# Kernel optimization log

Hardware: AMD Instinct MI355X
Metric: run time of the kernel (lower is better)

## Reference

```python
import jax, jax.numpy as jnp
import numpy as np

N = 100000
E = 1600000
H = 128
OUT = 16
NUM_GRAPHS = 64
BN_EPS = 1e-5


def setup_inputs() -> dict:
    key = jax.random.key(0)
    ks = jax.random.split(key, 16)
    x = jax.random.normal(ks[0], (N, 1), dtype=jnp.float32)
    edge_index = jax.random.randint(ks[1], (2, E), 0, N, dtype=jnp.int64)
    batch = jnp.sort(jax.random.randint(ks[2], (N,), 0, NUM_GRAPHS, dtype=jnp.int64))

    def glorot(k, shape):
        lim = float(np.sqrt(6.0 / (shape[0] + shape[1])))
        return jax.random.uniform(k, shape, jnp.float32, -lim, lim)

    return {
        "x": x, "edge_index": edge_index, "batch": batch,
        # conv 0: 1 -> H
        "W0": glorot(ks[3], (1, H)), "b0": jnp.zeros((H,), jnp.float32),
        "g0": jnp.ones((H,), jnp.float32), "beta0": jnp.zeros((H,), jnp.float32),
        # conv 1: H -> H
        "W1": glorot(ks[4], (H, H)), "b1": jnp.zeros((H,), jnp.float32),
        "g1": jnp.ones((H,), jnp.float32), "beta1": jnp.zeros((H,), jnp.float32),
        # conv 2: H -> H
        "W2": glorot(ks[5], (H, H)), "b2": jnp.zeros((H,), jnp.float32),
        "g2": jnp.ones((H,), jnp.float32), "beta2": jnp.zeros((H,), jnp.float32),
        # lin head
        "Wl": glorot(ks[6], (H, H)), "bl": jnp.zeros((H,), jnp.float32),
        "Wo": glorot(ks[7], (H, OUT)), "bo": jnp.zeros((OUT,), jnp.float32),
    }


def _gcn_norm(edge_index, n):
    # add self loops, symmetric normalization (PyG gcn_norm, edge_weight=1)
    loop = jnp.arange(n, dtype=edge_index.dtype)
    src = jnp.concatenate([edge_index[0], loop])
    dst = jnp.concatenate([edge_index[1], loop])
    deg = jax.ops.segment_sum(jnp.ones_like(src, jnp.float32), dst, num_segments=n)
    dis = jnp.where(deg > 0, jax.lax.rsqrt(deg), 0.0)
    return src, dst, dis[src] * dis[dst]


def _conv_bn_relu(h, src, dst, norm, n, W, b, g, beta):
    h = h @ W                                   # [N, H] linear transform first
    agg = jax.ops.segment_sum(h[src] * norm[:, None], dst, num_segments=n) + b
    m = agg.mean(axis=0)
    v = jnp.mean((agg - m) ** 2, axis=0)        # biased var (BN training mode)
    return jax.nn.relu(g * (agg - m) * jax.lax.rsqrt(v + BN_EPS) + beta)


def reference(x, edge_index, batch, W0, b0, g0, beta0, W1, b1, g1, beta1,
              W2, b2, g2, beta2, Wl, bl, Wo, bo):
    n = x.shape[0]
    src, dst, norm = _gcn_norm(edge_index, n)
    h = _conv_bn_relu(x, src, dst, norm, n, W0, b0, g0, beta0)
    h = _conv_bn_relu(h, src, dst, norm, n, W1, b1, g1, beta1)
    h = _conv_bn_relu(h, src, dst, norm, n, W2, b2, g2, beta2)
    # global mean pool per graph
    counts = jax.ops.segment_sum(jnp.ones((n,), h.dtype), batch, num_segments=NUM_GRAPHS)
    pooled = jax.ops.segment_sum(h, batch, num_segments=NUM_GRAPHS)
    pooled = pooled / jnp.maximum(counts, 1.0)[:, None]
    h = jax.nn.relu(pooled @ Wl + bl)
    return h @ Wo + bo
```

## Files before the change

### kernel.cpp

```cpp
#include <hip/hip_runtime.h>

#define HF 128
#define OUTF 16
#define NG 64
#define PBSH 7
#define PBSZ 128
#define CHUNK 4096
#define STAGE 4608
#define GBLK 2048
#define BN_EPS 1e-5f

typedef unsigned short ushortT;
typedef unsigned int uintT;
typedef unsigned char ucharT;
typedef __attribute__((ext_vector_type(8))) short bf16x8;
typedef __attribute__((ext_vector_type(4))) float f32x4;
typedef __attribute__((ext_vector_type(2))) float f32x2;

__device__ __forceinline__ float bf2f(uintT u) {
    union { uintT i; float f; } c; c.i = u << 16; return c.f;
}
__device__ __forceinline__ float bf2f_hi(uintT u) {
    union { uintT i; float f; } c; c.i = u & 0xffff0000u; return c.f;
}
__device__ __forceinline__ uintT f2bf(float f) {
    union { float f; uintT i; } c; c.f = f;
    uintT u = c.i;
    return (u + 0x7fffu + ((u >> 16) & 1u)) >> 16;
}
__device__ __forceinline__ uintT pack2(float a, float b) {
    return f2bf(a) | (f2bf(b) << 16);
}

__device__ __forceinline__ uintT fp8_enc2(float a, float b) {
    return (uintT)__builtin_amdgcn_cvt_pk_fp8_f32(a, b, 0, false) & 0xffffu;
}
__device__ __forceinline__ void fp8_acc8(float* a, uint2 v) {
    f32x2 f;
    f = __builtin_amdgcn_cvt_pk_f32_fp8((int)v.x, false); a[0] += f.x; a[1] += f.y;
    f = __builtin_amdgcn_cvt_pk_f32_fp8((int)v.x, true);  a[2] += f.x; a[3] += f.y;
    f = __builtin_amdgcn_cvt_pk_f32_fp8((int)v.y, false); a[4] += f.x; a[5] += f.y;
    f = __builtin_amdgcn_cvt_pk_f32_fp8((int)v.y, true);  a[6] += f.x; a[7] += f.y;
}


__global__ __launch_bounds__(1024) void bhist_kernel(const int* __restrict__ dst,
                                                     int* __restrict__ bhistB,
                                                     int E, int nbkt) {
    __shared__ int h[1024];
    int t = threadIdx.x, blk = blockIdx.x;
    if (t < 1024) h[t] = 0;
    __syncthreads();
    int e0 = blk * CHUNK, e1 = min(E, e0 + CHUNK);
    for (int e = e0 + t; e < e1; e += 1024) atomicAdd(&h[dst[e] >> PBSH], 1);
    __syncthreads();
    if (t < nbkt) bhistB[blk * 1024 + t] = h[t];
}

__global__ __launch_bounds__(256) void bscan_blocks_kernel(const int* __restrict__ bhistB,
                                                           int* __restrict__ lbase,
                                                           int* __restrict__ total,
                                                           int nblk, int nbkt) {
    int bkt = blockIdx.x * 4 + (threadIdx.x >> 6);
    int lane = threadIdx.x & 63;
    if (bkt >= nbkt) return;
    int run = 0;
    for (int base = 0; base < nblk; base += 64) {
        int blk = base + lane;
        int v = (blk < nblk) ? bhistB[(size_t)blk * 1024 + bkt] : 0;
        int pre = v;
        #pragma unroll
        for (int o = 1; o < 64; o <<= 1) {
            int u = __shfl_up(pre, o);
            if (lane >= o) pre += u;
        }
        if (blk < nblk) lbase[(size_t)blk * 1024 + bkt] = run + pre - v;
        run += __shfl(pre, 63);
    }
    if (lane == 0) total[bkt] = run;
}

__global__ __launch_bounds__(1024) void bscan_base_kernel(const int* __restrict__ total,
                                                          int* __restrict__ bbase, int nbkt) {
    __shared__ int sc[1024];
    int t = threadIdx.x;
    int v = (t < nbkt) ? total[t] : 0;
    sc[t] = v;
    __syncthreads();
    for (int o = 1; o < 1024; o <<= 1) {
        int add = (t >= o) ? sc[t - o] : 0;
        __syncthreads();
        sc[t] += add;
        __syncthreads();
    }
    if (t < nbkt) {
        bbase[t] = sc[t] - v;
        if (t == nbkt - 1) bbase[nbkt] = sc[t];
    }
}

__global__ __launch_bounds__(1024) void bscatter_kernel(const int* __restrict__ src,
                                                        const int* __restrict__ dst,
                                                        const int* __restrict__ bbase,
                                                        const int* __restrict__ lbase,
                                                        uintT* __restrict__ tmp,
                                                        int E, int nbkt) {
    __shared__ int cur[1024];
    int t = threadIdx.x, blk = blockIdx.x;
    if (t < nbkt) cur[t] = bbase[t] + lbase[(size_t)blk * 1024 + t];
    __syncthreads();
    int e0 = blk * CHUNK, e1 = min(E, e0 + CHUNK);
    for (int e = e0 + t; e < e1; e += 1024) {
        int d = dst[e];
        int bkt = d >> PBSH;
        int pos = atomicAdd(&cur[bkt], 1);
        tmp[pos] = ((uintT)(d & (PBSZ - 1)) << 18) | (uintT)src[e];
    }
}

__global__ __launch_bounds__(256) void breorder_kernel(const uintT* __restrict__ tmp,
                                                       const int* __restrict__ bbase,
                                                       const float* __restrict__ x,
                                                       int* __restrict__ rowptr,
                                                       int* __restrict__ csr_src,
                                                       float* __restrict__ dis,
                                                       float* __restrict__ xp,
                                                       int n, int nbkt) {
    __shared__ int lcnt[PBSZ];
    __shared__ int sc[PBSZ];
    __shared__ int lcur[PBSZ];
    __shared__ int stage[STAGE];
    int b = blockIdx.x, t = threadIdx.x;
    int n0 = b << PBSH;
    if (n0 >= n) return;
    int start = bbase[b], end = bbase[b + 1];
    int cnt = end - start;
    if (t < PBSZ) lcnt[t] = 0;
    __syncthreads();
    for (int i = t; i < cnt; i += 256) atomicAdd(&lcnt[tmp[start + i] >> 18], 1);
    __syncthreads();
    int v = (t < PBSZ) ? lcnt[t] : 0;
    if (t < PBSZ) sc[t] = v;
    __syncthreads();
    for (int o = 1; o < PBSZ; o <<= 1) {
        int add = (t < PBSZ && t >= o) ? sc[t - o] : 0;
        __syncthreads();
        if (t < PBSZ) sc[t] += add;
        __syncthreads();
    }
    if (t < PBSZ) {
        int pre = sc[t] - v;
        lcur[t] = pre;
        int node = n0 + t;
        if (node < n) {
            rowptr[node] = start + pre;
            float d = rsqrtf((float)v + 1.0f);
            dis[node] = d;
            xp[node] = d * x[node];
        }
    }
    if (b == nbkt - 1 && t == 0) rowptr[n] = end;
    __syncthreads();
    if (cnt <= STAGE) {
        for (int i = t; i < cnt; i += 256) {
            uintT p = tmp[start + i];
            int pos = atomicAdd(&lcur[p >> 18], 1);
            stage[pos] = (int)(p & 0x3ffffu);
        }
        __syncthreads();
        for (int i = t; i < cnt; i += 256) csr_src[start + i] = stage[i];
    } else {
        for (int i = t; i < cnt; i += 256) {
            uintT p = tmp[start + i];
            int pos = atomicAdd(&lcur[p >> 18], 1);
            csr_src[start + pos] = (int)(p & 0x3ffffu);
        }
    }
}


__global__ void gather1_kernel(const float* __restrict__ xp, const int* __restrict__ rowptr,
                               const int* __restrict__ csr_src, const float* __restrict__ dis,
                               float* __restrict__ aggx, int n) {
    int i = blockIdx.x * blockDim.x + threadIdx.x;
    if (i >= n) return;
    float acc = xp[i];
    int e = rowptr[i + 1];
    for (int j = rowptr[i]; j < e; ++j) acc += xp[csr_src[j]];
    aggx[i] = acc * dis[i];
}

__global__ void stats1_kernel(const float* __restrict__ aggx, float* __restrict__ stats1, int n) {
    float s = 0.f, ss = 0.f;
    for (int i = blockIdx.x * blockDim.x + threadIdx.x; i < n; i += gridDim.x * blockDim.x) {
        float v = aggx[i]; s += v; ss += v * v;
    }
    for (int o = 32; o > 0; o >>= 1) { s += __shfl_down(s, o); ss += __shfl_down(ss, o); }
    if ((threadIdx.x & 63) == 0) { atomicAdd(&stats1[0], s); atomicAdd(&stats1[1], ss); }
}

__global__ void coef0_kernel(const float* __restrict__ stats1, const float* __restrict__ W0,
                             const float* __restrict__ g, const float* __restrict__ beta,
                             float* __restrict__ coef, float invn) {
    int j = threadIdx.x;
    if (j < HF) {
        float m = stats1[0] * invn;
        float var = stats1[1] * invn - m * m;
        float w = W0[j];
        float sc = g[j] * w * rsqrtf(var * w * w + BN_EPS);
        coef[j] = sc;
        coef[HF + j] = beta[j] - m * sc;
    }
}


__global__ void wprep_kernel(const float* __restrict__ W, ushortT* __restrict__ Wt8) {
    int i = blockIdx.x * 256 + threadIdx.x;
    if (i >= 128 * 128) return;
    int k = i >> 7, j = i & 127;
    int byteoff = (j << 8) + ((k << 1) ^ ((j & 7) << 4));
    *(ushortT*)((char*)Wt8 + byteoff) = (ushortT)f2bf(W[i]);
}


__global__ __launch_bounds__(256) void gemm_mfma_kernel(const ushortT* __restrict__ A,
                                                        const float* __restrict__ aggx,
                                                        const ushortT* __restrict__ Wt8,
                                                        const float* __restrict__ coef,
                                                        const float* __restrict__ dis,
                                                        ucharT* __restrict__ C8, int n,
                                                        int mode) {
    __shared__ uint4 Wt[2048];
    int t = threadIdx.x;
    int wave = t >> 6, lane = t & 63;
    int l4 = lane >> 4;
    int lm = lane & 15;

    {
        const uint4* ws = reinterpret_cast<const uint4*>(Wt8);
        #pragma unroll
        for (int i = 0; i < 8; ++i) Wt[t + i * 256] = ws[t + i * 256];
    }
    __syncthreads();

    int rowBase = blockIdx.x * 64 + wave * 16;
    int ar = rowBase + lm;
    int arc = min(ar, n - 1);

    bf16x8 af[4];
    if (mode == 2) {
        float a = aggx[arc];
        #pragma unroll
        for (int kb = 0; kb < 4; ++kb) {
            int k0 = kb * 32 + l4 * 8;
            float4 sc0 = *reinterpret_cast<const float4*>(coef + k0);
            float4 sc1 = *reinterpret_cast<const float4*>(coef + k0 + 4);
            float4 sh0 = *reinterpret_cast<const float4*>(coef + HF + k0);
            float4 sh1 = *reinterpret_cast<const float4*>(coef + HF + k0 + 4);
            float scv[8] = {sc0.x, sc0.y, sc0.z, sc0.w, sc1.x, sc1.y, sc1.z, sc1.w};
            float shv[8] = {sh0.x, sh0.y, sh0.z, sh0.w, sh1.x, sh1.y, sh1.z, sh1.w};
            bf16x8 o;
            #pragma unroll
            for (int j = 0; j < 8; ++j) {
                float f = fmaxf(a * scv[j] + shv[j], 0.f);
                o[j] = (short)f2bf(f);
            }
            af[kb] = o;
        }
    } else {
        #pragma unroll
        for (int kb = 0; kb < 4; ++kb) {
            int k0 = kb * 32 + l4 * 8;
            bf16x8 v = *reinterpret_cast<const bf16x8*>(A + (size_t)arc * HF + k0);
            if (mode == 1) {
                float4 sc0 = *reinterpret_cast<const float4*>(coef + k0);
                float4 sc1 = *reinterpret_cast<const float4*>(coef + k0 + 4);
                float4 sh0 = *reinterpret_cast<const float4*>(coef + HF + k0);
                float4 sh1 = *reinterpret_cast<const float4*>(coef + HF + k0 + 4);
                float scv[8] = {sc0.x, sc0.y, sc0.z, sc0.w, sc1.x, sc1.y, sc1.z, sc1.w};
                float shv[8] = {sh0.x, sh0.y, sh0.z, sh0.w, sh1.x, sh1.y, sh1.z, sh1.w};
                bf16x8 o;
                #pragma unroll
                for (int j = 0; j < 8; ++j) {
                    float f = bf2f((uintT)(ushortT)v[j]);
                    f = fmaxf(f * scv[j] + shv[j], 0.f);
                    o[j] = (short)f2bf(f);
                }
                v = o;
            }
            af[kb] = v;
        }
    }

    f32x4 acc[8];
    #pragma unroll
    for (int ct = 0; ct < 8; ++ct) acc[ct] = (f32x4){0.f, 0.f, 0.f, 0.f};

    #pragma unroll
    for (int ct = 0; ct < 8; ++ct) {
        int col = ct * 16 + lm;
        int rowbyte = col << 8;
        int swz = (col & 7) << 4;
        #pragma unroll
        for (int kb = 0; kb < 4; ++kb) {
            int off = ((kb * 64 + l4 * 16) ^ swz);
            bf16x8 bf = *reinterpret_cast<const bf16x8*>((const char*)Wt + rowbyte + off);
            acc[ct] = __builtin_amdgcn_mfma_f32_16x16x32_bf16(af[kb], bf, acc[ct], 0, 0, 0);
        }
    }

    int rbase = rowBase + l4 * 4;
    float4 d4;
    if (rbase <= n - 4) {
        d4 = *reinterpret_cast<const float4*>(dis + rbase);
    } else {
        float tmp4[4];
        #pragma unroll
        for (int r = 0; r < 4; ++r) tmp4[r] = (rbase + r < n) ? dis[rbase + r] : 0.f;
        d4 = make_float4(tmp4[0], tmp4[1], tmp4[2], tmp4[3]);
    }
    const float* dd = (const float*)&d4;
    #pragma unroll
    for (int ct = 0; ct < 8; ++ct) {
        #pragma unroll
        for (int r = 0; r < 4; ++r) {
            float v = acc[ct][r] * dd[r];
            float o = __shfl_xor(v, 1);
            uintT pk = fp8_enc2(v, o);
            pk |= __shfl_xor(pk, 2) << 16;
            int row = rbase + r;
            if ((lane & 3) == 0 && row < n) {
                *(uintT*)(C8 + (size_t)row * HF + ct * 16 + lm) = pk;
            }
        }
    }
}


__global__ __launch_bounds__(256) void gather_stats_kernel(const ucharT* __restrict__ h8,
                                                           const int* __restrict__ rowptr,
                                                           const int* __restrict__ csr_src,
                                                           const float* __restrict__ dis,
                                                           ushortT* __restrict__ agg,
                                                           float* __restrict__ partial,
                                                           int n) {
    __shared__ float part[4][256];
    int t = threadIdx.x;
    int wave = t >> 6, lane = t & 63;
    int grp = lane >> 4;
    int l = lane & 15;
    float s[8], ss[8];
    #pragma unroll
    for (int i = 0; i < 8; ++i) { s[i] = 0.f; ss[i] = 0.f; }

    for (int node = blockIdx.x * 4 + wave; node < n; node += GBLK * 4) {
        int beg = rowptr[node], end = rowptr[node + 1];
        float a[8];
        #pragma unroll
        for (int i = 0; i < 8; ++i) a[i] = 0.f;
        if (grp == 0) {
            uint2 v = *reinterpret_cast<const uint2*>(h8 + (size_t)node * HF + l * 8);
            fp8_acc8(a, v);
        }
        for (int base = beg; base < end; base += 64) {
            int idx = base + lane;
            int sj = (idx < end) ? csr_src[idx] : 0;
            int cnt = min(64, end - base);
            for (int j = 0; j < cnt; j += 4) {
                int e = j + grp;
                int srcn = __shfl(sj, e < 64 ? e : 63);
                if (e < cnt) {
                    uint2 v = *reinterpret_cast<const uint2*>(h8 + (size_t)srcn * HF + l * 8);
                    fp8_acc8(a, v);
                }
            }
        }
        #pragma unroll
        for (int i = 0; i < 8; ++i) {
            a[i] += __shfl_xor(a[i], 16);
            a[i] += __shfl_xor(a[i], 32);
        }
        if (grp == 0) {
            float dd = dis[node];
            #pragma unroll
            for (int i = 0; i < 8; ++i) {
                a[i] *= dd;
                s[i] += a[i];
                ss[i] += a[i] * a[i];
            }
            uint4 o;
            o.x = pack2(a[0], a[1]);
            o.y = pack2(a[2], a[3]);
            o.z = pack2(a[4], a[5]);
            o.w = pack2(a[6], a[7]);
            *reinterpret_cast<uint4*>(agg + (size_t)node * HF + l * 8) = o;
        }
    }

    if (grp == 0) {
        #pragma unroll
        for (int i = 0; i < 8; ++i) {
            part[wave][l * 8 + i] = s[i];
            part[wave][128 + l * 8 + i] = ss[i];
        }
    }
    __syncthreads();
    float v = part[0][t] + part[1][t] + part[2][t] + part[3][t];
    partial[(size_t)blockIdx.x * 256 + t] = v;
}

__global__ __launch_bounds__(256) void reduce_stats_kernel(const float* __restrict__ partial,
                                                           float* __restrict__ stats, int nblk) {
    int t = threadIdx.x;
    float acc = 0.f;
    for (int b = blockIdx.x; b < nblk; b += gridDim.x) acc += partial[(size_t)b * 256 + t];
    atomicAdd(&stats[t], acc);
}

__global__ void bn_coef_kernel(const float* __restrict__ stats, const float* __restrict__ g,
                               const float* __restrict__ beta, float* __restrict__ coef,
                               float invn) {
    int j = threadIdx.x;
    if (j < HF) {
        float m = stats[j] * invn;
        float v = stats[HF + j] * invn - m * m;
        float sc = g[j] * rsqrtf(v + BN_EPS);
        coef[j] = sc;
        coef[HF + j] = beta[j] - m * sc;
    }
}


__global__ void starts_kernel(const int* __restrict__ batch, int* __restrict__ starts, int n) {
    int g = threadIdx.x;
    if (g > NG) return;
    int lo = 0, hi = n;
    while (lo < hi) {
        int mid = (lo + hi) >> 1;
        if (batch[mid] < g) lo = mid + 1; else hi = mid;
    }
    starts[g] = lo;
}

__global__ void pool_kernel(const ushortT* __restrict__ h, const float* __restrict__ coef,
                            const int* __restrict__ starts, float* __restrict__ pooled) {
    int g = blockIdx.x >> 4;
    int p = blockIdx.x & 15;
    int lane = threadIdx.x;
    float sc0 = coef[lane * 2],     sc1 = coef[lane * 2 + 1];
    float sh0 = coef[HF + lane * 2], sh1 = coef[HF + lane * 2 + 1];
    int s = starts[g], e = starts[g + 1];
    int len = e - s;
    int chunk = (len + 15) >> 4;
    int r0 = s + p * chunk;
    int r1 = min(e, r0 + chunk);
    float a0 = 0.f, a1 = 0.f;
    for (int r = r0; r < r1; ++r) {
        uintT v = *reinterpret_cast<const uintT*>(h + (size_t)r * HF + lane * 2);
        a0 += fmaxf(bf2f(v & 0xffff) * sc0 + sh0, 0.f);
        a1 += fmaxf(bf2f_hi(v) * sc1 + sh1, 0.f);
    }
    if (r1 > r0) {
        atomicAdd(&pooled[g * HF + lane * 2], a0);
        atomicAdd(&pooled[g * HF + lane * 2 + 1], a1);
    }
}


__global__ __launch_bounds__(1024) void head_kernel(const float* __restrict__ pooled,
                                                    const int* __restrict__ starts,
                                                    const float* __restrict__ Wl,
                                                    const float* __restrict__ bl,
                                                    const float* __restrict__ Wo,
                                                    const float* __restrict__ bo,
                                                    float* __restrict__ out) {
    __shared__ float P[NG][HF];
    __shared__ float T[NG][HF];
    int t = threadIdx.x;
    for (int i = t; i < NG * HF; i += 1024) {
        int g = i >> 7;
        float cnt = fmaxf((float)(starts[g + 1] - starts[g]), 1.0f);
        P[g][i & 127] = pooled[i] / cnt;
    }
    __syncthreads();
    for (int i = t; i < NG * HF; i += 1024) {
        int g = i >> 7, j = i & 127;
        float acc = bl[j];
        for (int k = 0; k < HF; ++k) acc += P[g][k] * Wl[k * HF + j];
        T[g][j] = fmaxf(acc, 0.f);
    }
    __syncthreads();
    int g = t >> 4, o = t & 15;
    float acc = bo[o];
    for (int k = 0; k < HF; ++k) acc += T[g][k] * Wo[k * OUTF + o];
    out[t] = acc;
}


extern "C" void kernel_launch(void* const* d_in, const int* in_sizes, int n_in,
                              void* d_out, int out_size, void* d_ws, size_t ws_size,
                              hipStream_t stream) {
    const float* x     = (const float*)d_in[0];
    const int*   ei    = (const int*)d_in[1];
    const int*   batch = (const int*)d_in[2];
    const float* W0 = (const float*)d_in[3];
    const float* g0 = (const float*)d_in[5];
    const float* be0 = (const float*)d_in[6];
    const float* W1 = (const float*)d_in[7];
    const float* g1 = (const float*)d_in[9];
    const float* be1 = (const float*)d_in[10];
    const float* W2 = (const float*)d_in[11];
    const float* g2 = (const float*)d_in[13];
    const float* be2 = (const float*)d_in[14];
    const float* Wl = (const float*)d_in[15];
    const float* bl = (const float*)d_in[16];
    const float* Wo = (const float*)d_in[17];
    const float* bo = (const float*)d_in[18];

    const int n = in_sizes[0];
    const int E = in_sizes[1] / 2;
    const int* srcI = ei;
    const int* dstI = ei + E;
    const int nbkt = (n + PBSZ - 1) >> PBSH;
    const int nblk = (E + CHUNK - 1) / CHUNK;

    ushortT* bufA = (ushortT*)d_ws;
    ushortT* bufB = bufA + (size_t)n * HF;
    ucharT* bufB8 = (ucharT*)bufB;
    float* dis    = (float*)(bufB + (size_t)n * HF);
    float* xp     = dis + n;
    float* aggx   = xp + n;
    float* stats  = aggx + n;
    float* coef   = stats + 2 * HF + 4;
    float* pooled = coef + 2 * HF;
    int* rowptr   = (int*)(pooled + NG * HF);
    int* csr_src  = rowptr + n + 1;
    uintT* tmp    = (uintT*)(csr_src + E);
    int* bhistB   = (int*)(tmp + E);
    int* lbase    = bhistB + (size_t)nblk * 1024;
    int* total    = lbase + (size_t)nblk * 1024;
    int* bbase    = total + 1024;
    int* starts   = bbase + 1025;
    float* partial = (float*)(starts + NG + 1);
    ushortT* wbuf = (ushortT*)(partial + (size_t)GBLK * 256);
    float* stats1 = stats + 2 * HF;

    bhist_kernel<<<nblk, 1024, 0, stream>>>(dstI, bhistB, E, nbkt);
    bscan_blocks_kernel<<<(nbkt + 3) / 4, 256, 0, stream>>>(bhistB, lbase, total, nblk, nbkt);
    bscan_base_kernel<<<1, 1024, 0, stream>>>(total, bbase, nbkt);
    bscatter_kernel<<<nblk, 1024, 0, stream>>>(srcI, dstI, bbase, lbase, tmp, E, nbkt);
    breorder_kernel<<<nbkt, 256, 0, stream>>>(tmp, bbase, x, rowptr, csr_src, dis, xp, n, nbkt);

    gather1_kernel<<<(n + 255) / 256, 256, 0, stream>>>(xp, rowptr, csr_src, dis, aggx, n);
    hipMemsetAsync(stats1, 0, 2 * 4, stream);
    stats1_kernel<<<256, 256, 0, stream>>>(aggx, stats1, n);
    coef0_kernel<<<1, 128, 0, stream>>>(stats1, W0, g0, be0, coef, 1.0f / n);

    wprep_kernel<<<64, 256, 0, stream>>>(W1, wbuf);
    gemm_mfma_kernel<<<(n + 63) / 64, 256, 0, stream>>>(bufA, aggx, wbuf, coef, dis, bufB8, n, 2);
    hipMemsetAsync(stats, 0, 256 * 4, stream);
    gather_stats_kernel<<<GBLK, 256, 0, stream>>>(bufB8, rowptr, csr_src, dis, bufA, partial, n);
    reduce_stats_kernel<<<128, 256, 0, stream>>>(partial, stats, GBLK);
    bn_coef_kernel<<<1, 128, 0, stream>>>(stats, g1, be1, coef, 1.0f / n);

    wprep_kernel<<<64, 256, 0, stream>>>(W2, wbuf);
    gemm_mfma_kernel<<<(n + 63) / 64, 256, 0, stream>>>(bufA, aggx, wbuf, coef, dis, bufB8, n, 1);
    hipMemsetAsync(stats, 0, 256 * 4, stream);
    gather_stats_kernel<<<GBLK, 256, 0, stream>>>(bufB8, rowptr, csr_src, dis, bufA, partial, n);
    reduce_stats_kernel<<<128, 256, 0, stream>>>(partial, stats, GBLK);
    bn_coef_kernel<<<1, 128, 0, stream>>>(stats, g2, be2, coef, 1.0f / n);

    starts_kernel<<<1, 128, 0, stream>>>(batch, starts, n);
    hipMemsetAsync(pooled, 0, NG * HF * 4, stream);
    pool_kernel<<<NG * 16, 64, 0, stream>>>(bufA, coef, starts, pooled);
    head_kernel<<<1, 1024, 0, stream>>>(pooled, starts, Wl, bl, Wo, bo, (float*)d_out);
}
```

Before: 326.5 us.

## Fuse CSR build into one cooperative kernel and cut launches and memsets

Result: slower. 484.8 us (+48.5%).

```diff
diff --git a/kernel.cpp b/kernel.cpp
--- a/kernel.cpp
+++ b/kernel.cpp
@@ -1,11 +1,15 @@
 #include <hip/hip_runtime.h>
+#include <hip/hip_cooperative_groups.h>
+
+namespace cg = cooperative_groups;
 
 #define HF 128
 #define OUTF 16
 #define NG 64
 #define PBSH 7
 #define PBSZ 128
-#define CHUNK 4096
+#define NBLKC 256
+#define MAXEPT 8
 #define STAGE 4608
 #define GBLK 2048
 #define BN_EPS 1e-5f
@@ -44,182 +48,203 @@
 }
 
 
-__global__ __launch_bounds__(1024) void bhist_kernel(const int* __restrict__ dst,
-                                                     int* __restrict__ bhistB,
-                                                     int E, int nbkt) {
+__global__ __launch_bounds__(1024) void csr_build_kernel(
+        const int* __restrict__ src, const int* __restrict__ dst,
+        const float* __restrict__ x,
+        int* __restrict__ bhistB, int* __restrict__ lbase,
+        int* __restrict__ total, int* __restrict__ bbase,
+        int* __restrict__ rowptr, int* __restrict__ csr_src,
+        float* __restrict__ dis, float* __restrict__ xp,
+        uintT* __restrict__ tmp,
+        int E, int n, int nbkt, int epb) {
+    cg::grid_group grid = cg::this_grid();
     __shared__ int h[1024];
-    int t = threadIdx.x, blk = blockIdx.x;
-    if (t < 1024) h[t] = 0;
-    __syncthreads();
-    int e0 = blk * CHUNK, e1 = min(E, e0 + CHUNK);
-    for (int e = e0 + t; e < e1; e += 1024) atomicAdd(&h[dst[e] >> PBSH], 1);
-    __syncthreads();
-    if (t < nbkt) bhistB[blk * 1024 + t] = h[t];
-}
-
-__global__ __launch_bounds__(256) void bscan_blocks_kernel(const int* __restrict__ bhistB,
-                                                           int* __restrict__ lbase,
-                                                           int* __restrict__ total,
-                                                           int nblk, int nbkt) {
-    int bkt = blockIdx.x * 4 + (threadIdx.x >> 6);
-    int lane = threadIdx.x & 63;
-    if (bkt >= nbkt) return;
-    int run = 0;
-    for (int base = 0; base < nblk; base += 64) {
-        int blk = base + lane;
-        int v = (blk < nblk) ? bhistB[(size_t)blk * 1024 + bkt] : 0;
-        int pre = v;
-        #pragma unroll
-        for (int o = 1; o < 64; o <<= 1) {
-            int u = __shfl_up(pre, o);
-            if (lane >= o) pre += u;
-        }
-        if (blk < nblk) lbase[(size_t)blk * 1024 + bkt] = run + pre - v;
-        run += __shfl(pre, 63);
-    }
-    if (lane == 0) total[bkt] = run;
-}
-
-__global__ __launch_bounds__(1024) void bscan_base_kernel(const int* __restrict__ total,
-                                                          int* __restrict__ bbase, int nbkt) {
-    __shared__ int sc[1024];
-    int t = threadIdx.x;
-    int v = (t < nbkt) ? total[t] : 0;
-    sc[t] = v;
-    __syncthreads();
-    for (int o = 1; o < 1024; o <<= 1) {
-        int add = (t >= o) ? sc[t - o] : 0;
-        __syncthreads();
-        sc[t] += add;
-        __syncthreads();
-    }
-    if (t < nbkt) {
-        bbase[t] = sc[t] - v;
-        if (t == nbkt - 1) bbase[nbkt] = sc[t];
-    }
-}
-
-__global__ __launch_bounds__(1024) void bscatter_kernel(const int* __restrict__ src,
-                                                        const int* __restrict__ dst,
-                                                        const int* __restrict__ bbase,
-                                                        const int* __restrict__ lbase,
-                                                        uintT* __restrict__ tmp,
-                                                        int E, int nbkt) {
-    __shared__ int cur[1024];
-    int t = threadIdx.x, blk = blockIdx.x;
-    if (t < nbkt) cur[t] = bbase[t] + lbase[(size_t)blk * 1024 + t];
-    __syncthreads();
-    int e0 = blk * CHUNK, e1 = min(E, e0 + CHUNK);
-    for (int e = e0 + t; e < e1; e += 1024) {
-        int d = dst[e];
-        int bkt = d >> PBSH;
-        int pos = atomicAdd(&cur[bkt], 1);
-        tmp[pos] = ((uintT)(d & (PBSZ - 1)) << 18) | (uintT)src[e];
-    }
-}
-
-__global__ __launch_bounds__(256) void breorder_kernel(const uintT* __restrict__ tmp,
-                                                       const int* __restrict__ bbase,
-                                                       const float* __restrict__ x,
-                                                       int* __restrict__ rowptr,
-                                                       int* __restrict__ csr_src,
-                                                       float* __restrict__ dis,
-                                                       float* __restrict__ xp,
-                                                       int n, int nbkt) {
     __shared__ int lcnt[PBSZ];
-    __shared__ int sc[PBSZ];
+    __shared__ int sc2[PBSZ];
     __shared__ int lcur[PBSZ];
     __shared__ int stage[STAGE];
-    int b = blockIdx.x, t = threadIdx.x;
-    int n0 = b << PBSH;
-    if (n0 >= n) return;
-    int start = bbase[b], end = bbase[b + 1];
-    int cnt = end - start;
-    if (t < PBSZ) lcnt[t] = 0;
-    __syncthreads();
-    for (int i = t; i < cnt; i += 256) atomicAdd(&lcnt[tmp[start + i] >> 18], 1);
-    __syncthreads();
-    int v = (t < PBSZ) ? lcnt[t] : 0;
-    if (t < PBSZ) sc[t] = v;
-    __syncthreads();
-    for (int o = 1; o < PBSZ; o <<= 1) {
-        int add = (t < PBSZ && t >= o) ? sc[t - o] : 0;
+
+    int t = threadIdx.x, blk = blockIdx.x;
+    int e0 = blk * epb;
+    int e1 = min(E, e0 + epb);
+
+    int es[MAXEPT], ed[MAXEPT];
+    h[t] = 0;
+    __syncthreads();
+    #pragma unroll
+    for (int k = 0; k < MAXEPT; ++k) {
+        int e = e0 + k * 1024 + t;
+        bool ok = e < e1;
+        es[k] = ok ? src[e] : -1;
+        ed[k] = ok ? dst[e] : -1;
+        if (ok) atomicAdd(&h[ed[k] >> PBSH], 1);
+    }
+    __syncthreads();
+    bhistB[(size_t)blk * 1024 + t] = h[t];
+    grid.sync();
+
+    {
+        int gw = blk * 16 + (t >> 6);
+        int lane = t & 63;
+        if (gw < nbkt) {
+            int run = 0;
+            for (int base = 0; base < NBLKC; base += 64) {
+                int b2 = base + lane;
+                int v = bhistB[(size_t)b2 * 1024 + gw];
+                int pre = v;
+                #pragma unroll
+                for (int o = 1; o < 64; o <<= 1) {
+                    int u = __shfl_up(pre, o);
+                    if (lane >= o) pre += u;
+                }
+                lbase[(size_t)b2 * 1024 + gw] = run + pre - v;
+                run += __shfl(pre, 63);
+            }
+            if (lane == 0) total[gw] = run;
+        }
+    }
+    grid.sync();
+
+    if (blk == 0) {
+        int v = (t < nbkt) ? total[t] : 0;
+        h[t] = v;
         __syncthreads();
-        if (t < PBSZ) sc[t] += add;
+        for (int o = 1; o < 1024; o <<= 1) {
+            int add = (t >= o) ? h[t - o] : 0;
+            __syncthreads();
+            h[t] += add;
+            __syncthreads();
+        }
+        if (t < nbkt) {
+            bbase[t] = h[t] - v;
+            if (t == nbkt - 1) bbase[nbkt] = h[t];
+        }
+    }
+    grid.sync();
+
+    if (t < nbkt) h[t] = bbase[t] + lbase[(size_t)blk * 1024 + t];
+    __syncthreads();
+    #pragma unroll
+    for (int k = 0; k < MAXEPT; ++k) {
+        if (ed[k] >= 0) {
+            int bkt = ed[k] >> PBSH;
+            int pos = atomicAdd(&h[bkt], 1);
+            tmp[pos] = ((uintT)(ed[k] & (PBSZ - 1)) << 18) | (uintT)es[k];
+        }
+    }
+    grid.sync();
+
+    for (int b = blk; b < nbkt; b += NBLKC) {
         __syncthreads();
-    }
-    if (t < PBSZ) {
-        int pre = sc[t] - v;
-        lcur[t] = pre;
-        int node = n0 + t;
-        if (node < n) {
-            rowptr[node] = start + pre;
-            float d = rsqrtf((float)v + 1.0f);
-            dis[node] = d;
-            xp[node] = d * x[node];
-        }
-    }
-    if (b == nbkt - 1 && t == 0) rowptr[n] = end;
-    __syncthreads();
-    if (cnt <= STAGE) {
-        for (int i = t; i < cnt; i += 256) {
-            uintT p = tmp[start + i];
-            int pos = atomicAdd(&lcur[p >> 18], 1);
-            stage[pos] = (int)(p & 0x3ffffu);
-        }
+        int n0 = b << PBSH;
+        if (n0 >= n) continue;
+        int start = bbase[b], end = bbase[b + 1];
+        int cnt = end - start;
+        if (t < PBSZ) lcnt[t] = 0;
         __syncthreads();
-        for (int i = t; i < cnt; i += 256) csr_src[start + i] = stage[i];
-    } else {
-        for (int i = t; i < cnt; i += 256) {
-            uintT p = tmp[start + i];
-            int pos = atomicAdd(&lcur[p >> 18], 1);
-            csr_src[start + pos] = (int)(p & 0x3ffffu);
-        }
-    }
-}
-
-
-__global__ void gather1_kernel(const float* __restrict__ xp, const int* __restrict__ rowptr,
-                               const int* __restrict__ csr_src, const float* __restrict__ dis,
-                               float* __restrict__ aggx, int n) {
-    int i = blockIdx.x * blockDim.x + threadIdx.x;
-    if (i >= n) return;
-    float acc = xp[i];
-    int e = rowptr[i + 1];
-    for (int j = rowptr[i]; j < e; ++j) acc += xp[csr_src[j]];
-    aggx[i] = acc * dis[i];
-}
-
-__global__ void stats1_kernel(const float* __restrict__ aggx, float* __restrict__ stats1, int n) {
+        for (int i = t; i < cnt; i += 1024) atomicAdd(&lcnt[tmp[start + i] >> 18], 1);
+        __syncthreads();
+        int v = (t < PBSZ) ? lcnt[t] : 0;
+        if (t < PBSZ) sc2[t] = v;
+        __syncthreads();
+        for (int o = 1; o < PBSZ; o <<= 1) {
+            int add = (t < PBSZ && t >= o) ? sc2[t - o] : 0;
+            __syncthreads();
+            if (t < PBSZ) sc2[t] += add;
+            __syncthreads();
+        }
+        if (t < PBSZ) {
+            int pre = sc2[t] - v;
+            lcur[t] = pre;
+            int node = n0 + t;
+            if (node < n) {
+                rowptr[node] = start + pre;
+                float d = rsqrtf((float)v + 1.0f);
+                dis[node] = d;
+                xp[node] = d * x[node];
+            }
+        }
+        if (b == nbkt - 1 && t == 0) rowptr[n] = end;
+        __syncthreads();
+        if (cnt <= STAGE) {
+            for (int i = t; i < cnt; i += 1024) {
+                uintT p = tmp[start + i];
+                int pos = atomicAdd(&lcur[p >> 18], 1);
+                stage[pos] = (int)(p & 0x3ffffu);
+            }
+            __syncthreads();
+            for (int i = t; i < cnt; i += 1024) csr_src[start + i] = stage[i];
+        } else {
+            for (int i = t; i < cnt; i += 1024) {
+                uintT p = tmp[start + i];
+                int pos = atomicAdd(&lcur[p >> 18], 1);
+                csr_src[start + pos] = (int)(p & 0x3ffffu);
+            }
+        }
+    }
+}
+
+
+__global__ __launch_bounds__(256) void gather1_kernel(const float* __restrict__ xp,
+                                                      const int* __restrict__ rowptr,
+                                                      const int* __restrict__ csr_src,
+                                                      const float* __restrict__ dis,
+                                                      float* __restrict__ aggx,
+                                                      float* __restrict__ partial1, int n) {
+    int t = threadIdx.x;
+    int i = blockIdx.x * 256 + t;
+    float v = 0.f;
+    if (i < n) {
+        float acc = xp[i];
+        int e = rowptr[i + 1];
+        for (int j = rowptr[i]; j < e; ++j) acc += xp[csr_src[j]];
+        v = acc * dis[i];
+        aggx[i] = v;
+    }
+    float s = v, ss = v * v;
+    for (int o = 32; o > 0; o >>= 1) { s += __shfl_down(s, o); ss += __shfl_down(ss, o); }
+    __shared__ float r2[2][4];
+    int wv = t >> 6, ln = t & 63;
+    if (ln == 0) { r2[0][wv] = s; r2[1][wv] = ss; }
+    __syncthreads();
+    if (t == 0) {
+        partial1[blockIdx.x * 2]     = r2[0][0] + r2[0][1] + r2[0][2] + r2[0][3];
+        partial1[blockIdx.x * 2 + 1] = r2[1][0] + r2[1][1] + r2[1][2] + r2[1][3];
+    }
+}
+
+__global__ void coef0_kernel(const float* __restrict__ partial1, int nblk1,
+                             const float* __restrict__ W0, const float* __restrict__ g,
+                             const float* __restrict__ beta, float* __restrict__ coef,
+                             float invn) {
+    __shared__ float rs[128], rss[128];
+    int t = threadIdx.x;
     float s = 0.f, ss = 0.f;
-    for (int i = blockIdx.x * blockDim.x + threadIdx.x; i < n; i += gridDim.x * blockDim.x) {
-        float v = aggx[i]; s += v; ss += v * v;
-    }
-    for (int o = 32; o > 0; o >>= 1) { s += __shfl_down(s, o); ss += __shfl_down(ss, o); }
-    if ((threadIdx.x & 63) == 0) { atomicAdd(&stats1[0], s); atomicAdd(&stats1[1], ss); }
-}
-
-__global__ void coef0_kernel(const float* __restrict__ stats1, const float* __restrict__ W0,
-                             const float* __restrict__ g, const float* __restrict__ beta,
-                             float* __restrict__ coef, float invn) {
-    int j = threadIdx.x;
-    if (j < HF) {
-        float m = stats1[0] * invn;
-        float var = stats1[1] * invn - m * m;
-        float w = W0[j];
-        float sc = g[j] * w * rsqrtf(var * w * w + BN_EPS);
-        coef[j] = sc;
-        coef[HF + j] = beta[j] - m * sc;
-    }
-}
-
-
-__global__ void wprep_kernel(const float* __restrict__ W, ushortT* __restrict__ Wt8) {
+    for (int k = t; k < nblk1; k += 128) { s += partial1[2 * k]; ss += partial1[2 * k + 1]; }
+    rs[t] = s; rss[t] = ss;
+    __syncthreads();
+    for (int o = 64; o > 0; o >>= 1) {
+        if (t < o) { rs[t] += rs[t + o]; rss[t] += rss[t + o]; }
+        __syncthreads();
+    }
+    float m = rs[0] * invn;
+    float var = rss[0] * invn - m * m;
+    float w = W0[t];
+    float sc = g[t] * w * rsqrtf(var * w * w + BN_EPS);
+    coef[t] = sc;
+    coef[HF + t] = beta[t] - m * sc;
+}
+
+
+__global__ void wprep2_kernel(const float* __restrict__ W1, const float* __restrict__ W2,
+                              ushortT* __restrict__ Wt1, ushortT* __restrict__ Wt2) {
     int i = blockIdx.x * 256 + threadIdx.x;
-    if (i >= 128 * 128) return;
-    int k = i >> 7, j = i & 127;
+    const float* W = (i < 16384) ? W1 : W2;
+    ushortT* Wt = (i < 16384) ? Wt1 : Wt2;
+    int ii = i & 16383;
+    int k = ii >> 7, j = ii & 127;
     int byteoff = (j << 8) + ((k << 1) ^ ((j & 7) << 4));
-    *(ushortT*)((char*)Wt8 + byteoff) = (ushortT)f2bf(W[i]);
+    *(ushortT*)((char*)Wt + byteoff) = (ushortT)f2bf(W[ii]);
 }
 
 
@@ -409,37 +434,46 @@
     partial[(size_t)blockIdx.x * 256 + t] = v;
 }
 
-__global__ __launch_bounds__(256) void reduce_stats_kernel(const float* __restrict__ partial,
-                                                           float* __restrict__ stats, int nblk) {
-    int t = threadIdx.x;
+__global__ __launch_bounds__(256) void reduce16_kernel(const float* __restrict__ partial,
+                                                       float* __restrict__ partial2, int nblk) {
+    int t = threadIdx.x, b = blockIdx.x;
     float acc = 0.f;
-    for (int b = blockIdx.x; b < nblk; b += gridDim.x) acc += partial[(size_t)b * 256 + t];
-    atomicAdd(&stats[t], acc);
-}
-
-__global__ void bn_coef_kernel(const float* __restrict__ stats, const float* __restrict__ g,
+    for (int r = b; r < nblk; r += 16) acc += partial[(size_t)r * 256 + t];
+    partial2[b * 256 + t] = acc;
+}
+
+__global__ void bn_coef_kernel(const float* __restrict__ partial2, const float* __restrict__ g,
                                const float* __restrict__ beta, float* __restrict__ coef,
                                float invn) {
-    int j = threadIdx.x;
-    if (j < HF) {
-        float m = stats[j] * invn;
-        float v = stats[HF + j] * invn - m * m;
-        float sc = g[j] * rsqrtf(v + BN_EPS);
-        coef[j] = sc;
-        coef[HF + j] = beta[j] - m * sc;
-    }
-}
-
-
-__global__ void starts_kernel(const int* __restrict__ batch, int* __restrict__ starts, int n) {
+    __shared__ float st[256];
+    int t = threadIdx.x;
+    float a = 0.f;
+    #pragma unroll
+    for (int b = 0; b < 16; ++b) a += partial2[b * 256 + t];
+    st[t] = a;
+    __syncthreads();
+    if (t < 128) {
+        float m = st[t] * invn;
+        float v = st[128 + t] * invn - m * m;
+        float sc = g[t] * rsqrtf(v + BN_EPS);
+        coef[t] = sc;
+        coef[HF + t] = beta[t] - m * sc;
+    }
+}
+
+
+__global__ void starts_kernel(const int* __restrict__ batch, int* __restrict__ starts,
+                              float* __restrict__ pooled, int n) {
     int g = threadIdx.x;
-    if (g > NG) return;
-    int lo = 0, hi = n;
-    while (lo < hi) {
-        int mid = (lo + hi) >> 1;
-        if (batch[mid] < g) lo = mid + 1; else hi = mid;
-    }
-    starts[g] = lo;
+    if (g <= NG) {
+        int lo = 0, hi = n;
+        while (lo < hi) {
+            int mid = (lo + hi) >> 1;
+            if (batch[mid] < g) lo = mid + 1; else hi = mid;
+        }
+        starts[g] = lo;
+    }
+    for (int i = threadIdx.x; i < NG * HF; i += 128) pooled[i] = 0.f;
 }
 
 __global__ void pool_kernel(const ushortT* __restrict__ h, const float* __restrict__ coef,
@@ -522,7 +556,8 @@
     const int* srcI = ei;
     const int* dstI = ei + E;
     const int nbkt = (n + PBSZ - 1) >> PBSH;
-    const int nblk = (E + CHUNK - 1) / CHUNK;
+    const int epb  = (E + NBLKC - 1) / NBLKC;
+    const int nblk1 = (n + 255) / 256;
 
     ushortT* bufA = (ushortT*)d_ws;
     ushortT* bufB = bufA + (size_t)n * HF;
@@ -530,48 +565,48 @@
     float* dis    = (float*)(bufB + (size_t)n * HF);
     float* xp     = dis + n;
     float* aggx   = xp + n;
-    float* stats  = aggx + n;
-    float* coef   = stats + 2 * HF + 4;
+    float* coef   = aggx + n;
     float* pooled = coef + 2 * HF;
     int* rowptr   = (int*)(pooled + NG * HF);
     int* csr_src  = rowptr + n + 1;
     uintT* tmp    = (uintT*)(csr_src + E);
     int* bhistB   = (int*)(tmp + E);
-    int* lbase    = bhistB + (size_t)nblk * 1024;
-    int* total    = lbase + (size_t)nblk * 1024;
+    int* lbase    = bhistB + (size_t)NBLKC * 1024;
+    int* total    = lbase + (size_t)NBLKC * 1024;
     int* bbase    = total + 1024;
     int* starts   = bbase + 1025;
     float* partial = (float*)(starts + NG + 1);
-    ushortT* wbuf = (ushortT*)(partial + (size_t)GBLK * 256);
-    float* stats1 = stats + 2 * HF;
-
-    bhist_kernel<<<nblk, 1024, 0, stream>>>(dstI, bhistB, E, nbkt);
-    bscan_blocks_kernel<<<(nbkt + 3) / 4, 256, 0, stream>>>(bhistB, lbase, total, nblk, nbkt);
-    bscan_base_kernel<<<1, 1024, 0, stream>>>(total, bbase, nbkt);
-    bscatter_kernel<<<nblk, 1024, 0, stream>>>(srcI, dstI, bbase, lbase, tmp, E, nbkt);
-    breorder_kernel<<<nbkt, 256, 0, stream>>>(tmp, bbase, x, rowptr, csr_src, dis, xp, n, nbkt);
-
-    gather1_kernel<<<(n + 255) / 256, 256, 0, stream>>>(xp, rowptr, csr_src, dis, aggx, n);
-    hipMemsetAsync(stats1, 0, 2 * 4, stream);
-    stats1_kernel<<<256, 256, 0, stream>>>(aggx, stats1, n);
-    coef0_kernel<<<1, 128, 0, stream>>>(stats1, W0, g0, be0, coef, 1.0f / n);
-
-    wprep_kernel<<<64, 256, 0, stream>>>(W1, wbuf);
-    gemm_mfma_kernel<<<(n + 63) / 64, 256, 0, stream>>>(bufA, aggx, wbuf, coef, dis, bufB8, n, 2);
-    hipMemsetAsync(stats, 0, 256 * 4, stream);
+    float* partial2 = partial + (size_t)GBLK * 256;
+    float* partial1 = partial2 + 16 * 256;
+    ushortT* wbuf1 = (ushortT*)(partial1 + (size_t)nblk1 * 2 + 2);
+    ushortT* wbuf2 = wbuf1 + 16384;
+
+    {
+        int E2 = E, n2 = n, nbkt2 = nbkt, epb2 = epb;
+        void* args[] = {(void*)&srcI, (void*)&dstI, (void*)&x,
+                        (void*)&bhistB, (void*)&lbase, (void*)&total, (void*)&bbase,
+                        (void*)&rowptr, (void*)&csr_src, (void*)&dis, (void*)&xp,
+                        (void*)&tmp, (void*)&E2, (void*)&n2, (void*)&nbkt2, (void*)&epb2};
+        hipLaunchCooperativeKernel((void*)csr_build_kernel, dim3(NBLKC), dim3(1024),
+                                   args, 0, stream);
+    }
+
+    gather1_kernel<<<nblk1, 256, 0, stream>>>(xp, rowptr, csr_src, dis, aggx, partial1, n);
+    coef0_kernel<<<1, 128, 0, stream>>>(partial1, nblk1, W0, g0, be0, coef, 1.0f / n);
+
+    wprep2_kernel<<<128, 256, 0, stream>>>(W1, W2, wbuf1, wbuf2);
+
+    gemm_mfma_kernel<<<(n + 63) / 64, 256, 0, stream>>>(bufA, aggx, wbuf1, coef, dis, bufB8, n, 2);
     gather_stats_kernel<<<GBLK, 256, 0, stream>>>(bufB8, rowptr, csr_src, dis, bufA, partial, n);
-    reduce_stats_kernel<<<128, 256, 0, stream>>>(partial, stats, GBLK);
-    bn_coef_kernel<<<1, 128, 0, stream>>>(stats, g1, be1, coef, 1.0f / n);
-
-    wprep_kernel<<<64, 256, 0, stream>>>(W2, wbuf);
-    gemm_mfma_kernel<<<(n + 63) / 64, 256, 0, stream>>>(bufA, aggx, wbuf, coef, dis, bufB8, n, 1);
-    hipMemsetAsync(stats, 0, 256 * 4, stream);
+    reduce16_kernel<<<16, 256, 0, stream>>>(partial, partial2, GBLK);
+    bn_coef_kernel<<<1, 256, 0, stream>>>(partial2, g1, be1, coef, 1.0f / n);
+
+    gemm_mfma_kernel<<<(n + 63) / 64, 256, 0, stream>>>(bufA, aggx, wbuf2, coef, dis, bufB8, n, 1);
     gather_stats_kernel<<<GBLK, 256, 0, stream>>>(bufB8, rowptr, csr_src, dis, bufA, partial, n);
-    reduce_stats_kernel<<<128, 256, 0, stream>>>(partial, stats, GBLK);
-    bn_coef_kernel<<<1, 128, 0, stream>>>(stats, g2, be2, coef, 1.0f / n);
-
-    starts_kernel<<<1, 128, 0, stream>>>(batch, starts, n);
-    hipMemsetAsync(pooled, 0, NG * HF * 4, stream);
+    reduce16_kernel<<<16, 256, 0, stream>>>(partial, partial2, GBLK);
+    bn_coef_kernel<<<1, 256, 0, stream>>>(partial2, g2, be2, coef, 1.0f / n);
+
+    starts_kernel<<<1, 128, 0, stream>>>(batch, starts, pooled, n);
     pool_kernel<<<NG * 16, 64, 0, stream>>>(bufA, coef, starts, pooled);
     head_kernel<<<1, 1024, 0, stream>>>(pooled, starts, Wl, bl, Wo, bo, (float*)d_out);
 }
```

## Cut launches and memsets by fusing stats reductions and weight prep

Applied to the files above, without the earlier changes.

After: 355.3 us. 8.8% more time.

```diff
diff --git a/kernel.cpp b/kernel.cpp
--- a/kernel.cpp
+++ b/kernel.cpp
@@ -179,47 +179,66 @@
 }
 
 
-__global__ void gather1_kernel(const float* __restrict__ xp, const int* __restrict__ rowptr,
-                               const int* __restrict__ csr_src, const float* __restrict__ dis,
-                               float* __restrict__ aggx, int n) {
-    int i = blockIdx.x * blockDim.x + threadIdx.x;
-    if (i >= n) return;
-    float acc = xp[i];
-    int e = rowptr[i + 1];
-    for (int j = rowptr[i]; j < e; ++j) acc += xp[csr_src[j]];
-    aggx[i] = acc * dis[i];
-}
-
-__global__ void stats1_kernel(const float* __restrict__ aggx, float* __restrict__ stats1, int n) {
+__global__ __launch_bounds__(256) void gather1_kernel(const float* __restrict__ xp,
+                                                      const int* __restrict__ rowptr,
+                                                      const int* __restrict__ csr_src,
+                                                      const float* __restrict__ dis,
+                                                      float* __restrict__ aggx,
+                                                      float* __restrict__ partial1, int n) {
+    int t = threadIdx.x;
+    int i = blockIdx.x * 256 + t;
+    float v = 0.f;
+    if (i < n) {
+        float acc = xp[i];
+        int e = rowptr[i + 1];
+        for (int j = rowptr[i]; j < e; ++j) acc += xp[csr_src[j]];
+        v = acc * dis[i];
+        aggx[i] = v;
+    }
+    float s = v, ss = v * v;
+    for (int o = 32; o > 0; o >>= 1) { s += __shfl_down(s, o); ss += __shfl_down(ss, o); }
+    __shared__ float r2[2][4];
+    int wv = t >> 6, ln = t & 63;
+    if (ln == 0) { r2[0][wv] = s; r2[1][wv] = ss; }
+    __syncthreads();
+    if (t == 0) {
+        partial1[blockIdx.x * 2]     = r2[0][0] + r2[0][1] + r2[0][2] + r2[0][3];
+        partial1[blockIdx.x * 2 + 1] = r2[1][0] + r2[1][1] + r2[1][2] + r2[1][3];
+    }
+}
+
+__global__ void coef0_kernel(const float* __restrict__ partial1, int nblk1,
+                             const float* __restrict__ W0, const float* __restrict__ g,
+                             const float* __restrict__ beta, float* __restrict__ coef,
+                             float invn) {
+    __shared__ float rs[128], rss[128];
+    int t = threadIdx.x;
     float s = 0.f, ss = 0.f;
-    for (int i = blockIdx.x * blockDim.x + threadIdx.x; i < n; i += gridDim.x * blockDim.x) {
-        float v = aggx[i]; s += v; ss += v * v;
-    }
-    for (int o = 32; o > 0; o >>= 1) { s += __shfl_down(s, o); ss += __shfl_down(ss, o); }
-    if ((threadIdx.x & 63) == 0) { atomicAdd(&stats1[0], s); atomicAdd(&stats1[1], ss); }
-}
-
-__global__ void coef0_kernel(const float* __restrict__ stats1, const float* __restrict__ W0,
-                             const float* __restrict__ g, const float* __restrict__ beta,
-                             float* __restrict__ coef, float invn) {
-    int j = threadIdx.x;
-    if (j < HF) {
-        float m = stats1[0] * invn;
-        float var = stats1[1] * invn - m * m;
-        float w = W0[j];
-        float sc = g[j] * w * rsqrtf(var * w * w + BN_EPS);
-        coef[j] = sc;
-        coef[HF + j] = beta[j] - m * sc;
-    }
-}
-
-
-__global__ void wprep_kernel(const float* __restrict__ W, ushortT* __restrict__ Wt8) {
+    for (int k = t; k < nblk1; k += 128) { s += partial1[2 * k]; ss += partial1[2 * k + 1]; }
+    rs[t] = s; rss[t] = ss;
+    __syncthreads();
+    for (int o = 64; o > 0; o >>= 1) {
+        if (t < o) { rs[t] += rs[t + o]; rss[t] += rss[t + o]; }
+        __syncthreads();
+    }
+    float m = rs[0] * invn;
+    float var = rss[0] * invn - m * m;
+    float w = W0[t];
+    float sc = g[t] * w * rsqrtf(var * w * w + BN_EPS);
+    coef[t] = sc;
+    coef[HF + t] = beta[t] - m * sc;
+}
+
+
+__global__ void wprep2_kernel(const float* __restrict__ W1, const float* __restrict__ W2,
+                              ushortT* __restrict__ Wt1, ushortT* __restrict__ Wt2) {
     int i = blockIdx.x * 256 + threadIdx.x;
-    if (i >= 128 * 128) return;
-    int k = i >> 7, j = i & 127;
+    const float* W = (i < 16384) ? W1 : W2;
+    ushortT* Wt = (i < 16384) ? Wt1 : Wt2;
+    int ii = i & 16383;
+    int k = ii >> 7, j = ii & 127;
     int byteoff = (j << 8) + ((k << 1) ^ ((j & 7) << 4));
-    *(ushortT*)((char*)Wt8 + byteoff) = (ushortT)f2bf(W[i]);
+    *(ushortT*)((char*)Wt + byteoff) = (ushortT)f2bf(W[ii]);
 }
 
 
@@ -409,37 +428,46 @@
     partial[(size_t)blockIdx.x * 256 + t] = v;
 }
 
-__global__ __launch_bounds__(256) void reduce_stats_kernel(const float* __restrict__ partial,
-                                                           float* __restrict__ stats, int nblk) {
-    int t = threadIdx.x;
+__global__ __launch_bounds__(256) void reduce16_kernel(const float* __restrict__ partial,
+                                                       float* __restrict__ partial2, int nblk) {
+    int t = threadIdx.x, b = blockIdx.x;
     float acc = 0.f;
-    for (int b = blockIdx.x; b < nblk; b += gridDim.x) acc += partial[(size_t)b * 256 + t];
-    atomicAdd(&stats[t], acc);
-}
-
-__global__ void bn_coef_kernel(const float* __restrict__ stats, const float* __restrict__ g,
+    for (int r = b; r < nblk; r += 16) acc += partial[(size_t)r * 256 + t];
+    partial2[b * 256 + t] = acc;
+}
+
+__global__ void bn_coef_kernel(const float* __restrict__ partial2, const float* __restrict__ g,
                                const float* __restrict__ beta, float* __restrict__ coef,
                                float invn) {
-    int j = threadIdx.x;
-    if (j < HF) {
-        float m = stats[j] * invn;
-        float v = stats[HF + j] * invn - m * m;
-        float sc = g[j] * rsqrtf(v + BN_EPS);
-        coef[j] = sc;
-        coef[HF + j] = beta[j] - m * sc;
-    }
-}
-
-
-__global__ void starts_kernel(const int* __restrict__ batch, int* __restrict__ starts, int n) {
+    __shared__ float st[256];
+    int t = threadIdx.x;
+    float a = 0.f;
+    #pragma unroll
+    for (int b = 0; b < 16; ++b) a += partial2[b * 256 + t];
+    st[t] = a;
+    __syncthreads();
+    if (t < 128) {
+        float m = st[t] * invn;
+        float v = st[128 + t] * invn - m * m;
+        float sc = g[t] * rsqrtf(v + BN_EPS);
+        coef[t] = sc;
+        coef[HF + t] = beta[t] - m * sc;
+    }
+}
+
+
+__global__ void starts_kernel(const int* __restrict__ batch, int* __restrict__ starts,
+                              float* __restrict__ pooled, int n) {
     int g = threadIdx.x;
-    if (g > NG) return;
-    int lo = 0, hi = n;
-    while (lo < hi) {
-        int mid = (lo + hi) >> 1;
-        if (batch[mid] < g) lo = mid + 1; else hi = mid;
-    }
-    starts[g] = lo;
+    if (g <= NG) {
+        int lo = 0, hi = n;
+        while (lo < hi) {
+            int mid = (lo + hi) >> 1;
+            if (batch[mid] < g) lo = mid + 1; else hi = mid;
+        }
+        starts[g] = lo;
+    }
+    for (int i = threadIdx.x; i < NG * HF; i += 128) pooled[i] = 0.f;
 }
 
 __global__ void pool_kernel(const ushortT* __restrict__ h, const float* __restrict__ coef,
@@ -523,6 +551,7 @@
     const int* dstI = ei + E;
     const int nbkt = (n + PBSZ - 1) >> PBSH;
     const int nblk = (E + CHUNK - 1) / CHUNK;
+    const int nblk1 = (n + 255) / 256;
 
     ushortT* bufA = (ushortT*)d_ws;
     ushortT* bufB = bufA + (size_t)n * HF;
@@ -530,8 +559,7 @@
     float* dis    = (float*)(bufB + (size_t)n * HF);
     float* xp     = dis + n;
     float* aggx   = xp + n;
-    float* stats  = aggx + n;
-    float* coef   = stats + 2 * HF + 4;
+    float* coef   = aggx + n;
     float* pooled = coef + 2 * HF;
     int* rowptr   = (int*)(pooled + NG * HF);
     int* csr_src  = rowptr + n + 1;
@@ -542,8 +570,10 @@
     int* bbase    = total + 1024;
     int* starts   = bbase + 1025;
     float* partial = (float*)(starts + NG + 1);
-    ushortT* wbuf = (ushortT*)(partial + (size_t)GBLK * 256);
-    float* stats1 = stats + 2 * HF;
+    float* partial2 = partial + (size_t)GBLK * 256;
+    float* partial1 = partial2 + 16 * 256;
+    ushortT* wbuf1 = (ushortT*)(partial1 + (size_t)nblk1 * 2 + 2);
+    ushortT* wbuf2 = wbuf1 + 16384;
 
     bhist_kernel<<<nblk, 1024, 0, stream>>>(dstI, bhistB, E, nbkt);
     bscan_blocks_kernel<<<(nbkt + 3) / 4, 256, 0, stream>>>(bhistB, lbase, total, nblk, nbkt);
@@ -551,27 +581,22 @@
     bscatter_kernel<<<nblk, 1024, 0, stream>>>(srcI, dstI, bbase, lbase, tmp, E, nbkt);
     breorder_kernel<<<nbkt, 256, 0, stream>>>(tmp, bbase, x, rowptr, csr_src, dis, xp, n, nbkt);
 
-    gather1_kernel<<<(n + 255) / 256, 256, 0, stream>>>(xp, rowptr, csr_src, dis, aggx, n);
-    hipMemsetAsync(stats1, 0, 2 * 4, stream);
-    stats1_kernel<<<256, 256, 0, stream>>>(aggx, stats1, n);
-    coef0_kernel<<<1, 128, 0, stream>>>(stats1, W0, g0, be0, coef, 1.0f / n);
-
-    wprep_kernel<<<64, 256, 0, stream>>>(W1, wbuf);
-    gemm_mfma_kernel<<<(n + 63) / 64, 256, 0, stream>>>(bufA, aggx, wbuf, coef, dis, bufB8, n, 2);
-    hipMemsetAsync(stats, 0, 256 * 4, stream);
+    gather1_kernel<<<nblk1, 256, 0, stream>>>(xp, rowptr, csr_src, dis, aggx, partial1, n);
+    coef0_kernel<<<1, 128, 0, stream>>>(partial1, nblk1, W0, g0, be0, coef, 1.0f / n);
+
+    wprep2_kernel<<<128, 256, 0, stream>>>(W1, W2, wbuf1, wbuf2);
+
+    gemm_mfma_kernel<<<(n + 63) / 64, 256, 0, stream>>>(bufA, aggx, wbuf1, coef, dis, bufB8, n, 2);
     gather_stats_kernel<<<GBLK, 256, 0, stream>>>(bufB8, rowptr, csr_src, dis, bufA, partial, n);
-    reduce_stats_kernel<<<128, 256, 0, stream>>>(partial, stats, GBLK);
-    bn_coef_kernel<<<1, 128, 0, stream>>>(stats, g1, be1, coef, 1.0f / n);
-
-    wprep_kernel<<<64, 256, 0, stream>>>(W2, wbuf);
-    gemm_mfma_kernel<<<(n + 63) / 64, 256, 0, stream>>>(bufA, aggx, wbuf, coef, dis, bufB8, n, 1);
-    hipMemsetAsync(stats, 0, 256 * 4, stream);
+    reduce16_kernel<<<16, 256, 0, stream>>>(partial, partial2, GBLK);
+    bn_coef_kernel<<<1, 256, 0, stream>>>(partial2, g1, be1, coef, 1.0f / n);
+
+    gemm_mfma_kernel<<<(n + 63) / 64, 256, 0, stream>>>(bufA, aggx, wbuf2, coef, dis, bufB8, n, 1);
     gather_stats_kernel<<<GBLK, 256, 0, stream>>>(bufB8, rowptr, csr_src, dis, bufA, partial, n);
-    reduce_stats_kernel<<<128, 256, 0, stream>>>(partial, stats, GBLK);
-    bn_coef_kernel<<<1, 128, 0, stream>>>(stats, g2, be2, coef, 1.0f / n);
-
-    starts_kernel<<<1, 128, 0, stream>>>(batch, starts, n);
-    hipMemsetAsync(pooled, 0, NG * HF * 4, stream);
+    reduce16_kernel<<<16, 256, 0, stream>>>(partial, partial2, GBLK);
+    bn_coef_kernel<<<1, 256, 0, stream>>>(partial2, g2, be2, coef, 1.0f / n);
+
+    starts_kernel<<<1, 128, 0, stream>>>(batch, starts, pooled, n);
     pool_kernel<<<NG * 16, 64, 0, stream>>>(bufA, coef, starts, pooled);
     head_kernel<<<1, 1024, 0, stream>>>(pooled, starts, Wl, bl, Wo, bo, (float*)d_out);
 }
```
